# Kernel tuning notes

Hardware: AMD Instinct MI355X
Metric: run time of the kernel (lower is better)

Reference implementation:

```python
import jax, jax.numpy as jnp
import numpy as np

VOCAB = 6
EPS = 1e-12


def _conv1d_same(x, w):
    # x: [B, Cin, L], w: [Cout, Cin, K] (odd K) -> [B, Cout, L]
    k = w.shape[-1]
    return jax.lax.conv_general_dilated(
        x, w, window_strides=(1,), padding=[(k // 2, k // 2)],
        dimension_numbers=("NCH", "OIH", "NCH"))


def setup_inputs() -> dict:
    key = jax.random.key(0)
    k1, k2, k3, k4 = jax.random.split(key, 4)
    B, L = 32, 2048
    Cin, Cout = VOCAB - 1, 256
    return {
        "input_ids": jax.random.randint(k1, (B, L), 0, VOCAB, dtype=jnp.int64),
        "attention_mask": jnp.ones((B, L), dtype=jnp.float32),
        "W3": jax.random.normal(k2, (Cout, Cin, 3), dtype=jnp.float32) * 0.1,
        "W5": jax.random.normal(k3, (Cout, Cin, 5), dtype=jnp.float32) * 0.1,
        "W7": jax.random.normal(k4, (Cout, Cin, 7), dtype=jnp.float32) * 0.1,
        "ln_gamma": jnp.ones((768,), dtype=jnp.float32),
        "ln_beta": jnp.zeros((768,), dtype=jnp.float32),
    }


def reference(input_ids, attention_mask, W3, W5, W7, ln_gamma, ln_beta):
    # One-hot over vocab, drop last class (padding token) -> [B, Cin, L]
    oh = jax.nn.one_hot(input_ids, VOCAB, dtype=jnp.float32)[:, :, : VOCAB - 1]
    x = jnp.transpose(oh, (0, 2, 1))  # [B, Cin, L]
    # Multi-kernel Conv1d, concat along channel dim -> [B, 768, L]
    h = jnp.concatenate([_conv1d_same(x, W3), _conv1d_same(x, W5), _conv1d_same(x, W7)], axis=1)
    # Zero out padded positions
    h = h * attention_mask[:, None, :]
    # [B, L, 768] then LayerNorm over last dim
    h = jnp.transpose(h, (0, 2, 1))
    mu = jnp.mean(h, axis=-1, keepdims=True)
    var = jnp.mean(jnp.square(h - mu), axis=-1, keepdims=True)
    out = (h - mu) * jax.lax.rsqrt(var + EPS) * ln_gamma + ln_beta
    return out  # dropout p=0.0 / eval mode -> identity
```

## Files before the change

kernel.cpp:

```cpp
#include <hip/hip_runtime.h>
#include <math.h>

namespace {

constexpr int kL       = 2048;
constexpr int kThreads = 512;
constexpr int kBlkPos  = 64;
constexpr int kPosPerWave = 8;

typedef float    vfloat4 __attribute__((ext_vector_type(4)));
typedef _Float16 half4   __attribute__((ext_vector_type(4)));
typedef _Float16 half2   __attribute__((ext_vector_type(2)));

template <int CTRL, int RM, bool BC>
__device__ __forceinline__ float dpp_step(float x) {
    return __int_as_float(__builtin_amdgcn_update_dpp(0, __float_as_int(x), CTRL, RM, 0xF, BC));
}

__device__ __forceinline__ void wave_sum2(float& x, float& y) {
    float tx, ty;
    tx = dpp_step<0xB1,  0xF, true >(x);  ty = dpp_step<0xB1,  0xF, true >(y);
    x += tx;                              y += ty;
    tx = dpp_step<0x4E,  0xF, true >(x);  ty = dpp_step<0x4E,  0xF, true >(y);
    x += tx;                              y += ty;
    tx = dpp_step<0x124, 0xF, true >(x);  ty = dpp_step<0x124, 0xF, true >(y);
    x += tx;                              y += ty;
    tx = dpp_step<0x128, 0xF, true >(x);  ty = dpp_step<0x128, 0xF, true >(y);
    x += tx;                              y += ty;
    tx = dpp_step<0x142, 0xA, false>(x);  ty = dpp_step<0x142, 0xA, false>(y);
    x += tx;                              y += ty;
    tx = dpp_step<0x143, 0xC, false>(x);  ty = dpp_step<0x143, 0xC, false>(y);
    x += tx;                              y += ty;
    x = __int_as_float(__builtin_amdgcn_readlane(__float_as_int(x), 63));
    y = __int_as_float(__builtin_amdgcn_readlane(__float_as_int(y), 63));
}

__device__ __forceinline__ half2 vlo(half4 v) { return __builtin_shufflevector(v, v, 0, 1); }
__device__ __forceinline__ half2 vhi(half4 v) { return __builtin_shufflevector(v, v, 2, 3); }

__device__ __forceinline__ int wrow(int t, int c) {
    return (c == 5) ? 75 : (t * 5 + c);
}

__global__ __launch_bounds__(kThreads, 8)
void cnn_emb_ln(const int*   __restrict__ ids,
                const float* __restrict__ mask,
                const float* __restrict__ W3,
                const float* __restrict__ W5,
                const float* __restrict__ W7,
                const float* __restrict__ gamma,
                const float* __restrict__ beta,
                float*       __restrict__ out)
{
    __shared__ half4 sW[76][64];

    const int tid  = threadIdx.x;
    const int lane = tid & 63;
    const int wave = tid >> 6;

    _Float16* sWh = reinterpret_cast<_Float16*>(sW);
    if (tid < 256) sWh[75 * 256 + tid] = (_Float16)0.f;

    {
        const float4* v4 = reinterpret_cast<const float4*>(W3);
        for (int i = tid; i < 960; i += kThreads) {
            const float4 v = v4[i];
            const float f[4] = {v.x, v.y, v.z, v.w};
            #pragma unroll
            for (int j = 0; j < 4; ++j) {
                const int e = 4 * i + j, o = e / 15, r = e % 15;
                sWh[((r % 3) * 5 + (r / 3)) * 256 + o] = (_Float16)f[j];
            }
        }
    }
    {
        const float4* v4 = reinterpret_cast<const float4*>(W5);
        for (int i = tid; i < 1600; i += kThreads) {
            const float4 v = v4[i];
            const float f[4] = {v.x, v.y, v.z, v.w};
            #pragma unroll
            for (int j = 0; j < 4; ++j) {
                const int e = 4 * i + j, o = e / 25, r = e % 25;
                sWh[((3 + r % 5) * 5 + (r / 5)) * 256 + o] = (_Float16)f[j];
            }
        }
    }
    {
        const float4* v4 = reinterpret_cast<const float4*>(W7);
        for (int i = tid; i < 2240; i += kThreads) {
            const float4 v = v4[i];
            const float f[4] = {v.x, v.y, v.z, v.w};
            #pragma unroll
            for (int j = 0; j < 4; ++j) {
                const int e = 4 * i + j, o = e / 35, r = e % 35;
                sWh[((8 + r % 7) * 5 + (r / 7)) * 256 + o] = (_Float16)f[j];
            }
        }
    }

    const int p0 = blockIdx.x * kBlkPos + wave * kPosPerWave;
    const int l0 = p0 & (kL - 1);

    int myc = 5;
    if (lane < kPosPerWave + 6) {
        const int lp = l0 - 3 + lane;
        if (lp >= 0 && lp < kL) {
            const int v = ids[p0 - 3 + lane];
            myc = (v < 5) ? v : 5;
        }
    }
    float mym = 0.f;
    if (lane < kPosPerWave) mym = mask[p0 + lane];

    half4 gh[3], bh[3];
    #pragma unroll
    for (int g = 0; g < 3; ++g) {
        const float4 gg = *reinterpret_cast<const float4*>(gamma + g * 256 + 4 * lane);
        const float4 bb = *reinterpret_cast<const float4*>(beta  + g * 256 + 4 * lane);
        gh[g] = half4{(_Float16)gg.x, (_Float16)gg.y, (_Float16)gg.z, (_Float16)gg.w};
        bh[g] = half4{(_Float16)bb.x, (_Float16)bb.y, (_Float16)bb.z, (_Float16)bb.w};
    }

    __syncthreads();

    const half2 ones = {(_Float16)1.f, (_Float16)1.f};
    const float inv_n = 1.0f / 768.0f;

    #pragma unroll
    for (int i = 0; i < kPosPerWave; ++i) {
        int c[7];
        #pragma unroll
        for (int j = 0; j < 7; ++j) c[j] = __builtin_amdgcn_readlane(myc, i + j);
        const float m = __int_as_float(__builtin_amdgcn_readlane(__float_as_int(mym), i));

        const half4 a3 =  sW[wrow(0, c[2])][lane] + sW[wrow(1, c[3])][lane]
                       +  sW[wrow(2, c[4])][lane];
        const half4 a5 = (sW[wrow(3, c[1])][lane] + sW[wrow(4, c[2])][lane])
                       + (sW[wrow(5, c[3])][lane] + sW[wrow(6, c[4])][lane])
                       +  sW[wrow(7, c[5])][lane];
        const half4 a7 = ((sW[wrow( 8, c[0])][lane] + sW[wrow( 9, c[1])][lane])
                       +  (sW[wrow(10, c[2])][lane] + sW[wrow(11, c[3])][lane]))
                       + ((sW[wrow(12, c[4])][lane] + sW[wrow(13, c[5])][lane])
                       +   sW[wrow(14, c[6])][lane]);

        float s = __builtin_amdgcn_fdot2(vlo(a3), ones, 0.f, false);
        s = __builtin_amdgcn_fdot2(vhi(a3), ones, s, false);
        s = __builtin_amdgcn_fdot2(vlo(a5), ones, s, false);
        s = __builtin_amdgcn_fdot2(vhi(a5), ones, s, false);
        s = __builtin_amdgcn_fdot2(vlo(a7), ones, s, false);
        s = __builtin_amdgcn_fdot2(vhi(a7), ones, s, false);
        float q = __builtin_amdgcn_fdot2(vlo(a3), vlo(a3), 0.f, false);
        q = __builtin_amdgcn_fdot2(vhi(a3), vhi(a3), q, false);
        q = __builtin_amdgcn_fdot2(vlo(a5), vlo(a5), q, false);
        q = __builtin_amdgcn_fdot2(vhi(a5), vhi(a5), q, false);
        q = __builtin_amdgcn_fdot2(vlo(a7), vlo(a7), q, false);
        q = __builtin_amdgcn_fdot2(vhi(a7), vhi(a7), q, false);

        wave_sum2(s, q);

        const float mu  = m * s * inv_n;
        const float ex2 = (m * m) * q * inv_n;
        const float var = fmaxf(ex2 - mu * mu, 0.0f);
        const float rs  = rsqrtf(var + 1e-12f);
        const float aa  = m * rs;
        const float cc  = -mu * rs;

        float* o = out + (size_t)(p0 + i) * 768 + 4 * lane;

        vfloat4 r;
        r.x = fmaf(fmaf((float)a3.x, aa, cc), (float)gh[0].x, (float)bh[0].x);
        r.y = fmaf(fmaf((float)a3.y, aa, cc), (float)gh[0].y, (float)bh[0].y);
        r.z = fmaf(fmaf((float)a3.z, aa, cc), (float)gh[0].z, (float)bh[0].z);
        r.w = fmaf(fmaf((float)a3.w, aa, cc), (float)gh[0].w, (float)bh[0].w);
        *reinterpret_cast<vfloat4*>(o) = r;

        r.x = fmaf(fmaf((float)a5.x, aa, cc), (float)gh[1].x, (float)bh[1].x);
        r.y = fmaf(fmaf((float)a5.y, aa, cc), (float)gh[1].y, (float)bh[1].y);
        r.z = fmaf(fmaf((float)a5.z, aa, cc), (float)gh[1].z, (float)bh[1].z);
        r.w = fmaf(fmaf((float)a5.w, aa, cc), (float)gh[1].w, (float)bh[1].w);
        *reinterpret_cast<vfloat4*>(o + 256) = r;

        r.x = fmaf(fmaf((float)a7.x, aa, cc), (float)gh[2].x, (float)bh[2].x);
        r.y = fmaf(fmaf((float)a7.y, aa, cc), (float)gh[2].y, (float)bh[2].y);
        r.z = fmaf(fmaf((float)a7.z, aa, cc), (float)gh[2].z, (float)bh[2].z);
        r.w = fmaf(fmaf((float)a7.w, aa, cc), (float)gh[2].w, (float)bh[2].w);
        *reinterpret_cast<vfloat4*>(o + 512) = r;
    }
}

}

extern "C" void kernel_launch(void* const* d_in, const int* in_sizes, int n_in,
                              void* d_out, int out_size, void* d_ws, size_t ws_size,
                              hipStream_t stream) {
    const int*   ids   = (const int*)  d_in[0];
    const float* mask  = (const float*)d_in[1];
    const float* W3    = (const float*)d_in[2];
    const float* W5    = (const float*)d_in[3];
    const float* W7    = (const float*)d_in[4];
    const float* gamma = (const float*)d_in[5];
    const float* beta  = (const float*)d_in[6];
    float*       out   = (float*)d_out;

    const int npos = in_sizes[0];
    const int grid = npos / kBlkPos;

    hipLaunchKernelGGL(cnn_emb_ln, dim3(grid), dim3(kThreads), 0, stream,
                       ids, mask, W3, W5, W7, gamma, beta, out);
}
```

Before: 43.72 us.

## Precompute fp16 weight table in separate kernel and read it from global memory

Adds a small prep kernel that builds a transposed fp16 weight lookup table in workspace. The main kernel then reads the table straight from global/L2 memory instead of having every block rebuild it in LDS, which removes the per-block staging and the __syncthreads. The block shrinks to 256 threads with 16 positions per wave, token offsets are held in a sliding register window, and gamma/beta stay in fp32. The cost is a second launch and gathers through the cache instead of LDS.

```diff
diff --git a/kernel.cpp b/kernel.cpp
--- a/kernel.cpp
+++ b/kernel.cpp
@@ -4,9 +4,9 @@
 namespace {
 
 constexpr int kL       = 2048;
-constexpr int kThreads = 512;
+constexpr int kThreads = 256;
+constexpr int kPosPerWave = 16;
 constexpr int kBlkPos  = 64;
-constexpr int kPosPerWave = 8;
 
 typedef float    vfloat4 __attribute__((ext_vector_type(4)));
 typedef _Float16 half4   __attribute__((ext_vector_type(4)));
@@ -38,65 +38,34 @@
 __device__ __forceinline__ half2 vlo(half4 v) { return __builtin_shufflevector(v, v, 0, 1); }
 __device__ __forceinline__ half2 vhi(half4 v) { return __builtin_shufflevector(v, v, 2, 3); }
 
-__device__ __forceinline__ int wrow(int t, int c) {
-    return (c == 5) ? 75 : (t * 5 + c);
+__global__ void prep_table(const float* __restrict__ W3,
+                           const float* __restrict__ W5,
+                           const float* __restrict__ W7,
+                           _Float16*    __restrict__ tb) {
+    const int g = blockIdx.x * blockDim.x + threadIdx.x;
+    if (g >= 90 * 256) return;
+    const int r = g >> 8, o = g & 255;
+    const int t = r / 6, c = r % 6;
+    float v = 0.f;
+    if (c < 5) {
+        if (t < 3)      v = W3[o * 15 + c * 3 + t];
+        else if (t < 8) v = W5[o * 25 + c * 5 + (t - 3)];
+        else            v = W7[o * 35 + c * 7 + (t - 8)];
+    }
+    tb[g] = (_Float16)v;
 }
 
-__global__ __launch_bounds__(kThreads, 8)
+__global__ __launch_bounds__(kThreads, 5)
 void cnn_emb_ln(const int*   __restrict__ ids,
                 const float* __restrict__ mask,
-                const float* __restrict__ W3,
-                const float* __restrict__ W5,
-                const float* __restrict__ W7,
+                const _Float16* __restrict__ tb,
                 const float* __restrict__ gamma,
                 const float* __restrict__ beta,
                 float*       __restrict__ out)
 {
-    __shared__ half4 sW[76][64];
-
     const int tid  = threadIdx.x;
     const int lane = tid & 63;
     const int wave = tid >> 6;
-
-    _Float16* sWh = reinterpret_cast<_Float16*>(sW);
-    if (tid < 256) sWh[75 * 256 + tid] = (_Float16)0.f;
-
-    {
-        const float4* v4 = reinterpret_cast<const float4*>(W3);
-        for (int i = tid; i < 960; i += kThreads) {
-            const float4 v = v4[i];
-            const float f[4] = {v.x, v.y, v.z, v.w};
-            #pragma unroll
-            for (int j = 0; j < 4; ++j) {
-                const int e = 4 * i + j, o = e / 15, r = e % 15;
-                sWh[((r % 3) * 5 + (r / 3)) * 256 + o] = (_Float16)f[j];
-            }
-        }
-    }
-    {
-        const float4* v4 = reinterpret_cast<const float4*>(W5);
-        for (int i = tid; i < 1600; i += kThreads) {
-            const float4 v = v4[i];
-            const float f[4] = {v.x, v.y, v.z, v.w};
-            #pragma unroll
-            for (int j = 0; j < 4; ++j) {
-                const int e = 4 * i + j, o = e / 25, r = e % 25;
-                sWh[((3 + r % 5) * 5 + (r / 5)) * 256 + o] = (_Float16)f[j];
-            }
-        }
-    }
-    {
-        const float4* v4 = reinterpret_cast<const float4*>(W7);
-        for (int i = tid; i < 2240; i += kThreads) {
-            const float4 v = v4[i];
-            const float f[4] = {v.x, v.y, v.z, v.w};
-            #pragma unroll
-            for (int j = 0; j < 4; ++j) {
-                const int e = 4 * i + j, o = e / 35, r = e % 35;
-                sWh[((8 + r % 7) * 5 + (r / 7)) * 256 + o] = (_Float16)f[j];
-            }
-        }
-    }
 
     const int p0 = blockIdx.x * kBlkPos + wave * kPosPerWave;
     const int l0 = p0 & (kL - 1);
@@ -112,36 +81,36 @@
     float mym = 0.f;
     if (lane < kPosPerWave) mym = mask[p0 + lane];
 
-    half4 gh[3], bh[3];
+    float ga[3][4], be[3][4];
     #pragma unroll
     for (int g = 0; g < 3; ++g) {
         const float4 gg = *reinterpret_cast<const float4*>(gamma + g * 256 + 4 * lane);
         const float4 bb = *reinterpret_cast<const float4*>(beta  + g * 256 + 4 * lane);
-        gh[g] = half4{(_Float16)gg.x, (_Float16)gg.y, (_Float16)gg.z, (_Float16)gg.w};
-        bh[g] = half4{(_Float16)bb.x, (_Float16)bb.y, (_Float16)bb.z, (_Float16)bb.w};
+        ga[g][0] = gg.x; ga[g][1] = gg.y; ga[g][2] = gg.z; ga[g][3] = gg.w;
+        be[g][0] = bb.x; be[g][1] = bb.y; be[g][2] = bb.z; be[g][3] = bb.w;
     }
 
-    __syncthreads();
-
+    const char* wb = reinterpret_cast<const char*>(tb);
+    const int lane8 = lane * 8;
     const half2 ones = {(_Float16)1.f, (_Float16)1.f};
     const float inv_n = 1.0f / 768.0f;
 
+    int a[7];
+    #pragma unroll
+    for (int j = 0; j < 7; ++j)
+        a[j] = (__builtin_amdgcn_readlane(myc, j) << 9) + lane8;
+
     #pragma unroll
     for (int i = 0; i < kPosPerWave; ++i) {
-        int c[7];
-        #pragma unroll
-        for (int j = 0; j < 7; ++j) c[j] = __builtin_amdgcn_readlane(myc, i + j);
         const float m = __int_as_float(__builtin_amdgcn_readlane(__float_as_int(mym), i));
 
-        const half4 a3 =  sW[wrow(0, c[2])][lane] + sW[wrow(1, c[3])][lane]
-                       +  sW[wrow(2, c[4])][lane];
-        const half4 a5 = (sW[wrow(3, c[1])][lane] + sW[wrow(4, c[2])][lane])
-                       + (sW[wrow(5, c[3])][lane] + sW[wrow(6, c[4])][lane])
-                       +  sW[wrow(7, c[5])][lane];
-        const half4 a7 = ((sW[wrow( 8, c[0])][lane] + sW[wrow( 9, c[1])][lane])
-                       +  (sW[wrow(10, c[2])][lane] + sW[wrow(11, c[3])][lane]))
-                       + ((sW[wrow(12, c[4])][lane] + sW[wrow(13, c[5])][lane])
-                       +   sW[wrow(14, c[6])][lane]);
+        #define RD(t, aj) (*reinterpret_cast<const half4*>(wb + (aj) + (t) * 3072))
+        const half4 a3 = (RD(0, a[2]) + RD(1, a[3])) + RD(2, a[4]);
+        const half4 a5 = ((RD(3, a[1]) + RD(4, a[2])) + (RD(5, a[3]) + RD(6, a[4])))
+                       + RD(7, a[5]);
+        const half4 a7 = ((RD(8, a[0]) + RD(9, a[1])) + (RD(10, a[2]) + RD(11, a[3])))
+                       + ((RD(12, a[4]) + RD(13, a[5])) + RD(14, a[6]));
+        #undef RD
 
         float s = __builtin_amdgcn_fdot2(vlo(a3), ones, 0.f, false);
         s = __builtin_amdgcn_fdot2(vhi(a3), ones, s, false);
@@ -168,23 +137,29 @@
         float* o = out + (size_t)(p0 + i) * 768 + 4 * lane;
 
         vfloat4 r;
-        r.x = fmaf(fmaf((float)a3.x, aa, cc), (float)gh[0].x, (float)bh[0].x);
-        r.y = fmaf(fmaf((float)a3.y, aa, cc), (float)gh[0].y, (float)bh[0].y);
-        r.z = fmaf(fmaf((float)a3.z, aa, cc), (float)gh[0].z, (float)bh[0].z);
-        r.w = fmaf(fmaf((float)a3.w, aa, cc), (float)gh[0].w, (float)bh[0].w);
+        r.x = fmaf(fmaf((float)a3.x, aa, cc), ga[0][0], be[0][0]);
+        r.y = fmaf(fmaf((float)a3.y, aa, cc), ga[0][1], be[0][1]);
+        r.z = fmaf(fmaf((float)a3.z, aa, cc), ga[0][2], be[0][2]);
+        r.w = fmaf(fmaf((float)a3.w, aa, cc), ga[0][3], be[0][3]);
         *reinterpret_cast<vfloat4*>(o) = r;
 
-        r.x = fmaf(fmaf((float)a5.x, aa, cc), (float)gh[1].x, (float)bh[1].x);
-        r.y = fmaf(fmaf((float)a5.y, aa, cc), (float)gh[1].y, (float)bh[1].y);
-        r.z = fmaf(fmaf((float)a5.z, aa, cc), (float)gh[1].z, (float)bh[1].z);
-        r.w = fmaf(fmaf((float)a5.w, aa, cc), (float)gh[1].w, (float)bh[1].w);
+        r.x = fmaf(fmaf((float)a5.x, aa, cc), ga[1][0], be[1][0]);
+        r.y = fmaf(fmaf((float)a5.y, aa, cc), ga[1][1], be[1][1]);
+        r.z = fmaf(fmaf((float)a5.z, aa, cc), ga[1][2], be[1][2]);
+        r.w = fmaf(fmaf((float)a5.w, aa, cc), ga[1][3], be[1][3]);
         *reinterpret_cast<vfloat4*>(o + 256) = r;
 
-        r.x = fmaf(fmaf((float)a7.x, aa, cc), (float)gh[2].x, (float)bh[2].x);
-        r.y = fmaf(fmaf((float)a7.y, aa, cc), (float)gh[2].y, (float)bh[2].y);
-        r.z = fmaf(fmaf((float)a7.z, aa, cc), (float)gh[2].z, (float)bh[2].z);
-        r.w = fmaf(fmaf((float)a7.w, aa, cc), (float)gh[2].w, (float)bh[2].w);
+        r.x = fmaf(fmaf((float)a7.x, aa, cc), ga[2][0], be[2][0]);
+        r.y = fmaf(fmaf((float)a7.y, aa, cc), ga[2][1], be[2][1]);
+        r.z = fmaf(fmaf((float)a7.z, aa, cc), ga[2][2], be[2][2]);
+        r.w = fmaf(fmaf((float)a7.w, aa, cc), ga[2][3], be[2][3]);
         *reinterpret_cast<vfloat4*>(o + 512) = r;
+
+        if (i < kPosPerWave - 1) {
+            #pragma unroll
+            for (int j = 0; j < 6; ++j) a[j] = a[j + 1];
+            a[6] = (__builtin_amdgcn_readlane(myc, i + 7) << 9) + lane8;
+        }
     }
 }
 
@@ -201,10 +176,13 @@
     const float* gamma = (const float*)d_in[5];
     const float* beta  = (const float*)d_in[6];
     float*       out   = (float*)d_out;
+    _Float16*    tb    = (_Float16*)d_ws;
+
+    hipLaunchKernelGGL(prep_table, dim3(90), dim3(256), 0, stream, W3, W5, W7, tb);
 
     const int npos = in_sizes[0];
     const int grid = npos / kBlkPos;
 
     hipLaunchKernelGGL(cnn_emb_ln, dim3(grid), dim3(kThreads), 0, stream,
-                       ids, mask, W3, W5, W7, gamma, beta, out);
+                       ids, mask, tb, gamma, beta, out);
 }
```

Result: slower. 48.87 us (+11.8%).
